# Optimization experiments

Hardware: AMD Instinct MI355X
Metric: run time of the kernel (lower is better)

The kernel has to match this reference:

```python
import jax, jax.numpy as jnp
import numpy as np

U = 64  # LSTM_UNITS

def _lstm(xt, kernel, rec, bias):
    # xt: [B, T, 4U]; keras LSTM gate order i, f, g(c), o
    B = xt.shape[0]
    h0 = jnp.zeros((B, U), xt.dtype)
    c0 = jnp.zeros((B, U), xt.dtype)
    def step(carry, x):
        h, c = carry
        z = x @ kernel + h @ rec + bias  # [B, 4U]
        i, f, g, o = jnp.split(z, 4, axis=-1)
        i = jax.nn.sigmoid(i); f = jax.nn.sigmoid(f)
        g = jnp.tanh(g); o = jax.nn.sigmoid(o)
        c = f * c + i * g
        h = o * jnp.tanh(c)
        return (h, c), h
    _, hs = jax.lax.scan(step, (h0, c0), jnp.swapaxes(xt, 0, 1))
    return jnp.swapaxes(hs, 0, 1)  # [B, T, U]

def setup_inputs() -> dict:
    key = jax.random.key(0)
    ks = jax.random.split(key, 12)
    B, T, P = 8, 100, 1000
    pro_id = jax.random.randint(ks[0], (B, T), 0, P, dtype=jnp.int32)
    label = jax.random.randint(ks[1], (B, T), 0, 2, dtype=jnp.int32)
    X = jax.random.normal(ks[2], (P, 2 * U), jnp.float32)
    cos_X = jax.random.uniform(ks[3], (P, P), jnp.float32)
    trimatrix = jnp.tril(jnp.ones((T, T), jnp.float32))  # causal mask [s, t]
    onehot_table = jax.random.normal(ks[4], (2, 4 * U), jnp.float32)
    s = 0.05
    lstm_kernel = jax.random.normal(ks[5], (4 * U, 4 * U), jnp.float32) * s
    lstm_rec = jax.random.normal(ks[6], (U, 4 * U), jnp.float32) * s
    lstm_bias = jnp.zeros((4 * U,), jnp.float32)
    W1 = jax.random.normal(ks[7], (3 * U, 50), jnp.float32) * s
    b1 = jnp.zeros((50,), jnp.float32)
    W2 = jax.random.normal(ks[8], (50, 1), jnp.float32) * s
    b2 = jnp.zeros((1,), jnp.float32)
    return {"pro_id": pro_id, "label": label, "num_pro": P, "X": X,
            "cos_X": cos_X, "trimatrix": trimatrix, "onehot_table": onehot_table,
            "lstm_kernel": lstm_kernel, "lstm_rec": lstm_rec, "lstm_bias": lstm_bias,
            "W1": W1, "b1": b1, "W2": W2, "b2": b2}

def reference(pro_id, label, num_pro, X, cos_X, trimatrix, onehot_table,
              lstm_kernel, lstm_rec, lstm_bias, W1, b1, W2, b2):
    B, T = pro_id.shape
    # one_hot @ X  ==  gather rows of X
    t_X = jnp.tile(X[pro_id], (1, 1, 2))           # [B, T, 4U]
    label_emb = onehot_table[label]                 # [B, T, 4U]
    xt = t_X * label_emb
    ht = _lstm(xt, lstm_kernel, lstm_rec, lstm_bias)  # [B, T, U]
    a = cos_X[pro_id]                               # [B, T, P] (one_hot @ cos_X)
    # ajhj[b,t,p,u] = sum_s tri[s,t] * a[b,s,p] * ht[b,s,u]  (causal weighted sum)
    ajhj = jnp.einsum('bsp,bsu,st->btpu', a, ht, trimatrix)
    XX = jnp.broadcast_to(X[None, None], (B, T, num_pro, 2 * U))
    hatt = jnp.concatenate([ajhj, XX], axis=-1)     # [B, T, P, 3U]
    r = jax.nn.relu(hatt @ W1 + b1)                 # [B, T, P, 50]
    prediction = r @ W2 + b2                        # [B, T, P, 1]
    return prediction
```

## Files before the change

kernel.cpp:

```cpp
#include <hip/hip_runtime.h>
#include <math.h>

#define BB 8
#define TT 100
#define PP 1000
#define NJ 52
#define GROW 56
#define HSTRIDE 68


__global__ __launch_bounds__(256) void k1_xk(const int* __restrict__ pro_id,
    const int* __restrict__ label, const float* __restrict__ X,
    const float* __restrict__ onehot, const float* __restrict__ kern,
    const float* __restrict__ bias, float* __restrict__ xk)
{
    __shared__ __align__(16) float xt[2][256];
    const int j = threadIdx.x;
    const int r0 = blockIdx.x * 2;
#pragma unroll
    for (int r = 0; r < 2; ++r) {
        int pid = pro_id[r0 + r];
        int lab = label[r0 + r];
        xt[r][j] = X[pid * 128 + (j & 127)] * onehot[lab * 256 + j];
    }
    __syncthreads();
    float acc0 = bias[j], acc1 = acc0;
    float kc[8];
#pragma unroll
    for (int i = 0; i < 8; ++i) kc[i] = kern[i * 256 + j];
    for (int kg = 0; kg < 32; ++kg) {
        float kn[8];
        const int kgn = (kg < 31) ? kg + 1 : 31;
#pragma unroll
        for (int i = 0; i < 8; ++i) kn[i] = kern[(kgn * 8 + i) * 256 + j];
        const int k0 = kg * 8;
        float4 xa0 = *(const float4*)&xt[0][k0];
        float4 xa1 = *(const float4*)&xt[0][k0 + 4];
        float4 xb0 = *(const float4*)&xt[1][k0];
        float4 xb1 = *(const float4*)&xt[1][k0 + 4];
        acc0 += xa0.x * kc[0] + xa0.y * kc[1] + xa0.z * kc[2] + xa0.w * kc[3]
              + xa1.x * kc[4] + xa1.y * kc[5] + xa1.z * kc[6] + xa1.w * kc[7];
        acc1 += xb0.x * kc[0] + xb0.y * kc[1] + xb0.z * kc[2] + xb0.w * kc[3]
              + xb1.x * kc[4] + xb1.y * kc[5] + xb1.z * kc[6] + xb1.w * kc[7];
#pragma unroll
        for (int i = 0; i < 8; ++i) kc[i] = kn[i];
    }
    xk[(r0 + 0) * 256 + j] = acc0;
    xk[(r0 + 1) * 256 + j] = acc1;
}

__global__ __launch_bounds__(256, 1) void mid(const float* __restrict__ xk,
    const float* __restrict__ rec, const float* __restrict__ W1,
    const float* __restrict__ X, const float* __restrict__ b1,
    float* __restrict__ G, float* __restrict__ XcT)
{
    __shared__ __align__(16) float smem[14720];
    const int tid = threadIdx.x;

    if (blockIdx.x < 8) {
        float* h_all = smem;
        float* w1s   = smem + (TT + 1) * HSTRIDE;
        const int b = blockIdx.x;
        const int l = tid & 63;
        const int w = tid >> 6;
        const int u = (w << 4) | (l & 15);
        const int g = l >> 4;
        const int col = (g << 6) | u;

        for (int idx = tid; idx < 3200; idx += 256) {
            int u2 = idx / 50, jj = idx - u2 * 50;
            w1s[u2 * 52 + jj] = W1[idx];
        }
        float rcol[64];
#pragma unroll
        for (int u2 = 0; u2 < 64; ++u2) rcol[u2] = rec[u2 * 256 + col];

        const float* xkb = xk + b * TT * 256;
        float xreg[TT];
#pragma unroll
        for (int t = 0; t < TT; ++t) xreg[t] = xkb[t * 256 + col];

        if (tid < 64) h_all[tid] = 0.f;
        float c = 0.f;
        __syncthreads();

#pragma unroll
        for (int t = 0; t < TT; ++t) {
            float a0 = xreg[t], a1 = 0.f, a2 = 0.f, a3 = 0.f;
            const float4* h4p = (const float4*)&h_all[t * HSTRIDE];
#pragma unroll
            for (int m = 0; m < 16; ++m) {
                float4 hv = h4p[m];
                a0 += hv.x * rcol[4 * m + 0];
                a1 += hv.y * rcol[4 * m + 1];
                a2 += hv.z * rcol[4 * m + 2];
                a3 += hv.w * rcol[4 * m + 3];
            }
            float z = (a0 + a1) + (a2 + a3);
            float act;
            if (g == 2) act = 2.f / (1.f + __expf(-2.f * z)) - 1.f;
            else        act = 1.f / (1.f + __expf(-z));
            const int base = l & 15;
            float gi = __shfl(act, base);
            float gf = __shfl(act, base + 16);
            float gg = __shfl(act, base + 32);
            float go = __shfl(act, base + 48);
            c = gf * c + gi * gg;
            float h = go * (2.f / (1.f + __expf(-2.f * c)) - 1.f);
            if (g == 0) h_all[(t + 1) * HSTRIDE + u] = h;
            __syncthreads();
        }

        const int brow0 = b * TT;
        for (int idx = tid; idx < TT * 13; idx += 256) {
            int row = idx / 13;
            int m = idx - row * 13;
            int j = 4 * m;
            const float* hrow = &h_all[(row + 1) * HSTRIDE];
            float ax = 0.f, ay = 0.f, az = 0.f, aw = 0.f;
#pragma unroll
            for (int u4 = 0; u4 < 16; ++u4) {
                float4 hv  = *(const float4*)&hrow[4 * u4];
                float4 w0  = *(const float4*)&w1s[(4 * u4 + 0) * 52 + j];
                float4 w1v = *(const float4*)&w1s[(4 * u4 + 1) * 52 + j];
                float4 w2  = *(const float4*)&w1s[(4 * u4 + 2) * 52 + j];
                float4 w3  = *(const float4*)&w1s[(4 * u4 + 3) * 52 + j];
                ax += hv.x * w0.x + hv.y * w1v.x + hv.z * w2.x + hv.w * w3.x;
                ay += hv.x * w0.y + hv.y * w1v.y + hv.z * w2.y + hv.w * w3.y;
                az += hv.x * w0.z + hv.y * w1v.z + hv.z * w2.z + hv.w * w3.z;
                aw += hv.x * w0.w + hv.y * w1v.w + hv.z * w2.w + hv.w * w3.w;
            }
            if (m == 12) { az = 0.f; aw = 0.f; }
            *(float4*)&G[(brow0 + row) * GROW + j] = make_float4(ax, ay, az, aw);
        }
    } else {
        float* Xs  = smem;
        float* W1T = smem + 8320;
        const int p0 = (blockIdx.x - 8) * 64;
        for (int idx = tid; idx < 6400; idx += 256) {
            int k = idx & 127, jj = idx >> 7;
            W1T[jj * 128 + k] = W1[(64 + k) * 50 + jj];
        }
#pragma unroll
        for (int r = 0; r < 8; ++r) {
            int flat = (tid + 256 * r) * 4;
            int i = flat >> 7;
            int k = flat & 127;
            int p = p0 + i;
            float4 v = make_float4(0.f, 0.f, 0.f, 0.f);
            if (p < PP) v = *(const float4*)&X[p * 128 + k];
            Xs[(k + 0) * 65 + i] = v.x;
            Xs[(k + 1) * 65 + i] = v.y;
            Xs[(k + 2) * 65 + i] = v.z;
            Xs[(k + 3) * 65 + i] = v.w;
        }
        __syncthreads();
        const int ploc = tid & 63;
        const int j0 = tid >> 6;
        float acc[13];
#pragma unroll
        for (int m = 0; m < 13; ++m) {
            int jj = j0 * 13 + m;
            acc[m] = (jj < 50) ? b1[jj] : 0.f;
        }
        for (int k4 = 0; k4 < 32; ++k4) {
            const int k = 4 * k4;
            float x0 = Xs[(k + 0) * 65 + ploc];
            float x1 = Xs[(k + 1) * 65 + ploc];
            float x2 = Xs[(k + 2) * 65 + ploc];
            float x3 = Xs[(k + 3) * 65 + ploc];
#pragma unroll
            for (int m = 0; m < 13; ++m) {
                int jj = j0 * 13 + m;
                if (jj < 50) {
                    float4 wv = *(const float4*)&W1T[jj * 128 + k];
                    acc[m] += x0 * wv.x + x1 * wv.y + x2 * wv.z + x3 * wv.w;
                }
            }
        }
        int p = p0 + ploc;
        if (p < PP) {
#pragma unroll
            for (int m = 0; m < 13; ++m) {
                int jj = j0 * 13 + m;
                if (jj < 50) XcT[jj * PP + p] = acc[m];
            }
        }
        for (int idx = tid; idx < 6 * 64; idx += 256) {
            int r = 50 + (idx >> 6);
            int pp = p0 + (idx & 63);
            if (pp < PP) XcT[r * PP + pp] = 0.f;
        }
    }
}

__global__ __launch_bounds__(256) void k4_main(const int* __restrict__ pro_id,
    const float* __restrict__ cos_X, const float* __restrict__ XcT,
    const float* __restrict__ G, const float* __restrict__ W2,
    const float* __restrict__ b2, float* __restrict__ out)
{
    __shared__ __align__(16) float Gs[TT * GROW];
    __shared__ float w2s[NJ];
    __shared__ int spid[TT];
    const int b = blockIdx.z;
    const int p = blockIdx.y * 256 + threadIdx.x;
    const int ci = blockIdx.x;
    const int t0 = ci * 7;
    const int t1 = (t0 + 7 < TT) ? (t0 + 7) : TT;
    const bool valid = p < PP;
    const int pc = valid ? p : 0;
    const int tid = threadIdx.x;

    {
        const float4* Gg = (const float4*)(G + b * TT * GROW);
        float4* Gd = (float4*)Gs;
        for (int idx = tid; idx < TT * GROW / 4; idx += 256) Gd[idx] = Gg[idx];
        if (tid < TT) spid[tid] = pro_id[b * TT + tid];
        if (tid < NJ) w2s[tid] = (tid < 50) ? W2[tid] : 0.f;
    }

    float V[NJ];
#pragma unroll
    for (int jj = 0; jj < NJ; ++jj) V[jj] = XcT[jj * PP + pc];
    const float b2v = b2[0];
    __syncthreads();

    const float* cb = cos_X + pc;
    float a0 = cb[spid[99] * PP];
    float a1 = cb[spid[98] * PP];
    float a2 = cb[spid[97] * PP];
    float a3 = cb[spid[96] * PP];

    for (int s = TT - 1; s >= t0; --s) {
        float a = a0; a0 = a1; a1 = a2; a2 = a3;
        int sp = s - 4;
        if (sp < t0) sp = t0;
        a3 = cb[spid[sp] * PP];
        const float4* G4 = (const float4*)&Gs[s * GROW];
#pragma unroll
        for (int jv = 0; jv < 13; ++jv) {
            float4 gv = G4[jv];
            V[4 * jv + 0] += a * gv.x;
            V[4 * jv + 1] += a * gv.y;
            V[4 * jv + 2] += a * gv.z;
            V[4 * jv + 3] += a * gv.w;
        }
        if (s < t1) {
            float acc = b2v;
#pragma unroll
            for (int jv = 0; jv < 13; ++jv) {
                float4 wv = *(const float4*)&w2s[4 * jv];
                acc += wv.x * fmaxf(V[4 * jv + 0], 0.f)
                     + wv.y * fmaxf(V[4 * jv + 1], 0.f)
                     + wv.z * fmaxf(V[4 * jv + 2], 0.f)
                     + wv.w * fmaxf(V[4 * jv + 3], 0.f);
            }
            if (valid) out[(b * TT + s) * PP + p] = acc;
        }
    }
}

extern "C" void kernel_launch(void* const* d_in, const int* in_sizes, int n_in,
                              void* d_out, int out_size, void* d_ws, size_t ws_size,
                              hipStream_t stream)
{
    const int* pro_id  = (const int*)d_in[0];
    const int* label   = (const int*)d_in[1];
    const float* X     = (const float*)d_in[3];
    const float* cos_X = (const float*)d_in[4];
    const float* onehot = (const float*)d_in[6];
    const float* lk    = (const float*)d_in[7];
    const float* lr    = (const float*)d_in[8];
    const float* lb    = (const float*)d_in[9];
    const float* W1    = (const float*)d_in[10];
    const float* b1    = (const float*)d_in[11];
    const float* W2    = (const float*)d_in[12];
    const float* b2    = (const float*)d_in[13];

    float* ws  = (float*)d_ws;
    float* xk  = ws;
    float* XcT = ws + 204800;
    float* G   = ws + 260800;
    float* out = (float*)d_out;

    hipLaunchKernelGGL(k1_xk,  dim3(400),      dim3(256), 0, stream,
                       pro_id, label, X, onehot, lk, lb, xk);
    hipLaunchKernelGGL(mid,    dim3(24),       dim3(256), 0, stream,
                       xk, lr, W1, X, b1, G, XcT);
    hipLaunchKernelGGL(k4_main,dim3(15, 4, 8), dim3(256), 0, stream,
                       pro_id, cos_X, XcT, G, W2, b2, out);
}
```

Baseline: 210.0 us.

## Run LSTM recurrence in a single wavefront with fp16 dot2 and no barriers

The LSTM recurrence now runs in a single 64-lane wavefront, with each lane computing all four gates of one unit. This removes the per-timestep __syncthreads and the cross-lane shuffles. The recurrent weights are packed to fp16 pairs in registers and multiplied with v_dot2 against an fp16 copy of h, and xk inputs are prefetched three steps ahead. The other waves load W1 in parallel. It depends on implicit wavefront lockstep for the shared hwork buffer, and the fp16 rounding of h and rec adds precision error.

```diff
diff --git a/kernel.cpp b/kernel.cpp
--- a/kernel.cpp
+++ b/kernel.cpp
@@ -6,7 +6,12 @@
 #define PP 1000
 #define NJ 52
 #define GROW 56
-#define HSTRIDE 68
+
+typedef _Float16 half2v __attribute__((ext_vector_type(2)));
+
+__device__ __forceinline__ half2v as_h2(float f) {
+    union { float x; half2v h; } u; u.x = f; return u.h;
+}
 
 
 __global__ __launch_bounds__(256) void k1_xk(const int* __restrict__ pro_id,
@@ -58,65 +63,91 @@
     const int tid = threadIdx.x;
 
     if (blockIdx.x < 8) {
-        float* h_all = smem;
-        float* w1s   = smem + (TT + 1) * HSTRIDE;
+        float* h_all  = smem;
+        float* hwork  = smem + 6400;
+        float* w1s    = smem + 6432;
         const int b = blockIdx.x;
-        const int l = tid & 63;
-        const int w = tid >> 6;
-        const int u = (w << 4) | (l & 15);
-        const int g = l >> 4;
-        const int col = (g << 6) | u;
-
-        for (int idx = tid; idx < 3200; idx += 256) {
-            int u2 = idx / 50, jj = idx - u2 * 50;
-            w1s[u2 * 52 + jj] = W1[idx];
-        }
-        float rcol[64];
-#pragma unroll
-        for (int u2 = 0; u2 < 64; ++u2) rcol[u2] = rec[u2 * 256 + col];
-
-        const float* xkb = xk + b * TT * 256;
-        float xreg[TT];
-#pragma unroll
-        for (int t = 0; t < TT; ++t) xreg[t] = xkb[t * 256 + col];
-
-        if (tid < 64) h_all[tid] = 0.f;
-        float c = 0.f;
+
+        if (tid >= 64) {
+            for (int idx = tid - 64; idx < 3200; idx += 192) {
+                int u2 = idx / 50, jj = idx - u2 * 50;
+                w1s[u2 * 52 + jj] = W1[idx];
+            }
+        }
+
+        if (tid < 64) {
+            const int u = tid;
+            half2v rp[4][32];
+#pragma unroll
+            for (int m = 0; m < 32; ++m) {
+#pragma unroll
+                for (int g2 = 0; g2 < 4; ++g2) {
+                    float r0 = rec[(2 * m) * 256 + g2 * 64 + u];
+                    float r1 = rec[(2 * m + 1) * 256 + g2 * 64 + u];
+                    half2v pv; pv.x = (_Float16)r0; pv.y = (_Float16)r1;
+                    rp[g2][m] = pv;
+                }
+            }
+            ((_Float16*)hwork)[u] = (_Float16)0.f;
+
+            const float* xkb = xk + b * TT * 256;
+            float xi0 = xkb[u],           xf0 = xkb[64 + u],
+                  xg0 = xkb[128 + u],     xo0 = xkb[192 + u];
+            float xi1 = xkb[256 + u],     xf1 = xkb[256 + 64 + u],
+                  xg1 = xkb[256 + 128 + u], xo1 = xkb[256 + 192 + u];
+            float xi2 = xkb[512 + u],     xf2 = xkb[512 + 64 + u],
+                  xg2 = xkb[512 + 128 + u], xo2 = xkb[512 + 192 + u];
+            float c = 0.f;
+
+            for (int t = 0; t < TT; ++t) {
+                float zi = xi0, zf = xf0, zg = xg0, zo = xo0;
+                xi0 = xi1; xf0 = xf1; xg0 = xg1; xo0 = xo1;
+                xi1 = xi2; xf1 = xf2; xg1 = xg2; xo1 = xo2;
+                int tn = (t + 3 < TT) ? t + 3 : TT - 1;
+                const float* xp = xkb + tn * 256;
+                xi2 = xp[u]; xf2 = xp[64 + u]; xg2 = xp[128 + u]; xo2 = xp[192 + u];
+
+                const float4* hw4 = (const float4*)hwork;
+#pragma unroll
+                for (int ch = 0; ch < 8; ++ch) {
+                    float4 hv = hw4[ch];
+                    half2v p0 = as_h2(hv.x), p1 = as_h2(hv.y),
+                           p2 = as_h2(hv.z), p3 = as_h2(hv.w);
+                    zi = __builtin_amdgcn_fdot2(p0, rp[0][ch * 4 + 0], zi, false);
+                    zf = __builtin_amdgcn_fdot2(p0, rp[1][ch * 4 + 0], zf, false);
+                    zg = __builtin_amdgcn_fdot2(p0, rp[2][ch * 4 + 0], zg, false);
+                    zo = __builtin_amdgcn_fdot2(p0, rp[3][ch * 4 + 0], zo, false);
+                    zi = __builtin_amdgcn_fdot2(p1, rp[0][ch * 4 + 1], zi, false);
+                    zf = __builtin_amdgcn_fdot2(p1, rp[1][ch * 4 + 1], zf, false);
+                    zg = __builtin_amdgcn_fdot2(p1, rp[2][ch * 4 + 1], zg, false);
+                    zo = __builtin_amdgcn_fdot2(p1, rp[3][ch * 4 + 1], zo, false);
+                    zi = __builtin_amdgcn_fdot2(p2, rp[0][ch * 4 + 2], zi, false);
+                    zf = __builtin_amdgcn_fdot2(p2, rp[1][ch * 4 + 2], zf, false);
+                    zg = __builtin_amdgcn_fdot2(p2, rp[2][ch * 4 + 2], zg, false);
+                    zo = __builtin_amdgcn_fdot2(p2, rp[3][ch * 4 + 2], zo, false);
+                    zi = __builtin_amdgcn_fdot2(p3, rp[0][ch * 4 + 3], zi, false);
+                    zf = __builtin_amdgcn_fdot2(p3, rp[1][ch * 4 + 3], zf, false);
+                    zg = __builtin_amdgcn_fdot2(p3, rp[2][ch * 4 + 3], zg, false);
+                    zo = __builtin_amdgcn_fdot2(p3, rp[3][ch * 4 + 3], zo, false);
+                }
+                float gi = 1.f / (1.f + __expf(-zi));
+                float gf = 1.f / (1.f + __expf(-zf));
+                float gg = 2.f / (1.f + __expf(-2.f * zg)) - 1.f;
+                float go = 1.f / (1.f + __expf(-zo));
+                c = gf * c + gi * gg;
+                float h = go * (2.f / (1.f + __expf(-2.f * c)) - 1.f);
+                h_all[t * 64 + u] = h;
+                ((_Float16*)hwork)[u] = (_Float16)h;
+            }
+        }
         __syncthreads();
-
-#pragma unroll
-        for (int t = 0; t < TT; ++t) {
-            float a0 = xreg[t], a1 = 0.f, a2 = 0.f, a3 = 0.f;
-            const float4* h4p = (const float4*)&h_all[t * HSTRIDE];
-#pragma unroll
-            for (int m = 0; m < 16; ++m) {
-                float4 hv = h4p[m];
-                a0 += hv.x * rcol[4 * m + 0];
-                a1 += hv.y * rcol[4 * m + 1];
-                a2 += hv.z * rcol[4 * m + 2];
-                a3 += hv.w * rcol[4 * m + 3];
-            }
-            float z = (a0 + a1) + (a2 + a3);
-            float act;
-            if (g == 2) act = 2.f / (1.f + __expf(-2.f * z)) - 1.f;
-            else        act = 1.f / (1.f + __expf(-z));
-            const int base = l & 15;
-            float gi = __shfl(act, base);
-            float gf = __shfl(act, base + 16);
-            float gg = __shfl(act, base + 32);
-            float go = __shfl(act, base + 48);
-            c = gf * c + gi * gg;
-            float h = go * (2.f / (1.f + __expf(-2.f * c)) - 1.f);
-            if (g == 0) h_all[(t + 1) * HSTRIDE + u] = h;
-            __syncthreads();
-        }
 
         const int brow0 = b * TT;
         for (int idx = tid; idx < TT * 13; idx += 256) {
             int row = idx / 13;
             int m = idx - row * 13;
             int j = 4 * m;
-            const float* hrow = &h_all[(row + 1) * HSTRIDE];
+            const float* hrow = &h_all[row * 64];
             float ax = 0.f, ay = 0.f, az = 0.f, aw = 0.f;
 #pragma unroll
             for (int u4 = 0; u4 < 16; ++u4) {
```

Measured after the change: 198.5 us. 5.5% less time.
